# Kernel tuning notes

Hardware: AMD Instinct MI355X
Metric: run time of the kernel (lower is better)

The kernel has to match this reference:

```python
import jax, jax.numpy as jnp
import numpy as np
from jax import lax

DEPTH = 3
KS = 5

def haar_fwd(x):
    # x: (B, 2h, 2w, C) -> (B, h, w, C, 4) with bands [LL, LH, HL, HH]
    a = x[:, 0::2, 0::2]; b = x[:, 0::2, 1::2]
    c = x[:, 1::2, 0::2]; d = x[:, 1::2, 1::2]
    ll = (a + b + c + d) * 0.5
    lh = (a + b - c - d) * 0.5
    hl = (a - b + c - d) * 0.5
    hh = (a - b - c + d) * 0.5
    return jnp.stack([ll, lh, hl, hh], axis=-1)

def haar_inv(co):
    # co: (B, h, w, C, 4) -> (B, 2h, 2w, C); orthonormal inverse of haar_fwd
    ll, lh, hl, hh = co[..., 0], co[..., 1], co[..., 2], co[..., 3]
    a = (ll + lh + hl + hh) * 0.5
    b = (ll + lh - hl - hh) * 0.5
    c = (ll - lh + hl - hh) * 0.5
    d = (ll - lh - hl + hh) * 0.5
    B, h, w, C = ll.shape
    top = jnp.stack([a, b], axis=3).reshape(B, h, 2 * w, C)
    bot = jnp.stack([c, d], axis=3).reshape(B, h, 2 * w, C)
    return jnp.stack([top, bot], axis=2).reshape(B, 2 * h, 2 * w, C)

def depthwise(x, k, groups):
    return lax.conv_general_dilated(
        x, k, (1, 1), 'SAME',
        dimension_numbers=('NHWC', 'HWIO', 'NHWC'),
        feature_group_count=groups)

def setup_inputs() -> dict:
    key = jax.random.key(0)
    ks = jax.random.split(key, 2 + DEPTH)
    B, H, W, C = 8, 256, 256, 128
    x = jax.random.normal(ks[0], (B, H, W, C), jnp.float32)
    fan = float(KS * KS)
    base_kernel = jax.random.normal(ks[1], (KS, KS, 1, C), jnp.float32) / np.sqrt(fan)
    base_bias = jnp.zeros((C,), jnp.float32)
    base_scale = jnp.ones((1, 1, 1, C), jnp.float32)
    wavelet_kernels = tuple(
        jax.random.normal(ks[2 + i], (KS, KS, 1, C * 4), jnp.float32) / np.sqrt(fan)
        for i in range(DEPTH))
    wavelet_scales = tuple(jnp.full((1, 1, 1, C * 4), 0.1, jnp.float32) for _ in range(DEPTH))
    return dict(x=x, base_kernel=base_kernel, base_bias=base_bias, base_scale=base_scale,
                wavelet_kernels=wavelet_kernels, wavelet_scales=wavelet_scales)

def reference(x, base_kernel, base_bias, base_scale, wavelet_kernels, wavelet_scales):
    B, H, W, C = x.shape
    # pad input to even H/W (edge mode); no-op for even dims
    xp = jnp.pad(x, ((0, 0), (0, H % 2), (0, W % 2), (0, 0)), mode='edge')
    # multi-level Haar forward: level l decomposes the raw LL of level l-1
    coeffs, dims = [], []
    cur = xp
    for _ in range(DEPTH):
        _, h, w, _ = cur.shape
        dims.append((h, w))
        cur = jnp.pad(cur, ((0, 0), (0, h % 2), (0, w % 2), (0, 0)), mode='edge')
        co = haar_fwd(cur)
        coeffs.append(co)
        cur = co[..., 0]
    # per-level depthwise conv with scale fused into the kernel
    conv_coeffs = []
    for lvl in range(DEPTH):
        co = coeffs[lvl]
        Bc, h, w, Cc, _ = co.shape
        flat = co.reshape(Bc, h, w, Cc * 4)
        fused = wavelet_scales[lvl] * wavelet_kernels[lvl]  # (KS,KS,1,4C)
        out = depthwise(flat, fused, Cc * 4)
        conv_coeffs.append(out.reshape(Bc, h, w, Cc, 4))
    # inverse reconstruction with add of deeper reconstruction into LL band
    next_ll = jnp.zeros_like(conv_coeffs[-1][..., 0])
    for lvl in range(DEPTH - 1, -1, -1):
        co = conv_coeffs[lvl].at[..., 0].add(next_ll)
        rec = haar_inv(co)
        h, w = dims[lvl]
        next_ll = rec[:, :h, :w, :]
    output_wt = next_ll[:, :H, :W, :]
    x_base = base_scale * (depthwise(xp, base_kernel, C) + base_bias)[:, :H, :W, :]
    return x_base + output_wt
```

## Files before the change

kernel.cpp:

```cpp
#include <hip/hip_runtime.h>

#define NC 128
#define NB 8
#define CPB 32

__device__ __forceinline__ float4 ld4(const float* p) { return *(const float4*)p; }
__device__ __forceinline__ float4 add4(float4 a, float4 b) {
    return make_float4(a.x + b.x, a.y + b.y, a.z + b.z, a.w + b.w);
}
__device__ __forceinline__ float4 sub4(float4 a, float4 b) {
    return make_float4(a.x - b.x, a.y - b.y, a.z - b.z, a.w - b.w);
}
__device__ __forceinline__ float4 muls4(float4 a, float s) {
    return make_float4(a.x * s, a.y * s, a.z * s, a.w * s);
}
__device__ __forceinline__ float4 fma4(float4 a, float4 w, float4 c) {
    return make_float4(fmaf(a.x, w.x, c.x), fmaf(a.y, w.y, c.y),
                       fmaf(a.z, w.z, c.z), fmaf(a.w, w.w, c.w));
}

__global__ __launch_bounds__(256) void k_haar_ll(
    const float* __restrict__ P, float* __restrict__ out, int h, int w)
{
    int idx = blockIdx.x * blockDim.x + threadIdx.x;
    int total = NB * h * w * (NC / 4);
    if (idx >= total) return;
    int cq = idx & (NC / 4 - 1);
    int t  = idx / (NC / 4);
    int j  = t % w; t /= w;
    int i  = t % h;
    int b  = t / h;
    size_t W2C  = (size_t)(2 * w) * NC;
    size_t base = (((size_t)b * (2 * h) + 2 * i) * (2 * w) + 2 * j) * NC + cq * 4;
    float4 A  = *(const float4*)(P + base);
    float4 Bv = *(const float4*)(P + base + NC);
    float4 Cv = *(const float4*)(P + base + W2C);
    float4 Dv = *(const float4*)(P + base + W2C + NC);
    float4 r;
    r.x = (A.x + Bv.x + Cv.x + Dv.x) * 0.5f;
    r.y = (A.y + Bv.y + Cv.y + Dv.y) * 0.5f;
    r.z = (A.z + Bv.z + Cv.z + Dv.z) * 0.5f;
    r.w = (A.w + Bv.w + Cv.w + Dv.w) * 0.5f;
    *(float4*)(out + (size_t)idx * 4) = r;
}

#define WL4(s, t)  (wl + ((s) * 25 + (t)) * CPB + 4 * tc)
#define WB4(m, n)  (wbase + ((m) * 5 + (n)) * CPB + 4 * tc)

template <bool BASE, int RR>
__global__ __launch_bounds__(256) void k_convinv(
    const float* __restrict__ P, const float* __restrict__ nll,
    const float* __restrict__ wk, const float* __restrict__ wsc,
    const float* __restrict__ bk, const float* __restrict__ bb,
    const float* __restrict__ bs, float* __restrict__ out,
    int h, int w)
{
    extern __shared__ float lds[];
    float* wl     = lds;
    float* wbase  = wl + 4 * 25 * CPB;
    float* bscale = wbase + 25 * CPB;
    float* bbias  = bscale + CPB;

    const int cg    = blockIdx.x & 3;
    const int jtile = blockIdx.x >> 2;
    const int c0    = cg * CPB;
    const int tid   = threadIdx.x + threadIdx.y * 8;

    for (int u = tid; u < 4 * 25 * CPB; u += 256) {
        int tcc = u & (CPB - 1);
        int st  = u / CPB;
        int t   = st % 25;
        int s   = st / 25;
        wl[u] = 0.5f * wsc[(c0 + tcc) * 4 + s] * wk[t * (4 * NC) + (c0 + tcc) * 4 + s];
    }
    if (BASE) {
        for (int u = tid; u < 25 * CPB; u += 256) {
            int tcc = u & (CPB - 1);
            int t   = u / CPB;
            wbase[u] = bk[t * NC + c0 + tcc];
        }
        if (tid < CPB) { bscale[tid] = bs[c0 + tid]; bbias[tid] = bb[c0 + tid]; }
    }
    __syncthreads();

    const int tc = threadIdx.x;
    const int cc = c0 + 4 * tc;
    const int b  = blockIdx.z;
    const int i  = blockIdx.y;
    const int ja = jtile * (32 * RR) + threadIdx.y * RR;
    if (ja >= w) return;
    const int PH = 2 * h;
    const size_t rowC = (size_t)(2 * w) * NC;

    int   coff[RR + 4];
    float cmask[RR + 4];
    #pragma unroll
    for (int q = 0; q < RR + 4; ++q) {
        int xq  = ja + q - 2;
        int xqc = min(max(xq, 0), w - 1);
        coff[q]  = xqc * (2 * NC);
        cmask[q] = (xq >= 0 && xq < w) ? 1.f : 0.f;
    }

    float4 acc0[RR], acc1[RR], acc2[RR], acc3[RR];
    float4 b00[RR], b01[RR], b10[RR], b11[RR];
    #pragma unroll
    for (int s = 0; s < RR; ++s) {
        acc0[s] = acc1[s] = acc2[s] = acc3[s] = make_float4(0.f, 0.f, 0.f, 0.f);
        b00[s] = b01[s] = b10[s] = b11[s] = make_float4(0.f, 0.f, 0.f, 0.f);
    }

    #pragma unroll
    for (int ky = 0; ky < 5; ++ky) {
        int y = i + ky - 2;
        if (y < 0 || y >= h) continue;
        const float* prA = P + ((size_t)b * PH + 2 * y) * rowC + cc;
        const float* prC = prA + rowC;
        #pragma unroll
        for (int q = 0; q < RR + 4; ++q) {
            float m = cmask[q];
            const float* pA = prA + coff[q];
            const float* pC = prC + coff[q];
            float4 A  = muls4(ld4(pA), m);
            float4 Bv = muls4(ld4(pA + NC), m);
            float4 Cv = muls4(ld4(pC), m);
            float4 Dv = muls4(ld4(pC + NC), m);
            float4 sA = add4(A, Bv), sC = add4(Cv, Dv);
            float4 dA = sub4(A, Bv), dC = sub4(Cv, Dv);
            float4 s0 = add4(sA, sC), s1 = sub4(sA, sC);
            float4 s2 = add4(dA, dC), s3 = sub4(dA, dC);
            #pragma unroll
            for (int s = 0; s < RR; ++s) {
                const int kx = q - s;
                if (kx < 0 || kx > 4) continue;
                const int t = ky * 5 + kx;
                acc0[s] = fma4(s0, ld4(WL4(0, t)), acc0[s]);
                acc1[s] = fma4(s1, ld4(WL4(1, t)), acc1[s]);
                acc2[s] = fma4(s2, ld4(WL4(2, t)), acc2[s]);
                acc3[s] = fma4(s3, ld4(WL4(3, t)), acc3[s]);
                if (BASE && ky >= 1 && ky <= 3 && kx >= 1 && kx <= 3) {
                    b00[s] = fma4(A, ld4(WB4(2 * ky - 2, 2 * kx - 2)), b00[s]);
                    if (kx >= 2)            b01[s] = fma4(A,  ld4(WB4(2 * ky - 2, 2 * kx - 3)), b01[s]);
                    if (ky >= 2)            b10[s] = fma4(A,  ld4(WB4(2 * ky - 3, 2 * kx - 2)), b10[s]);
                    if (ky >= 2 && kx >= 2) b11[s] = fma4(A,  ld4(WB4(2 * ky - 3, 2 * kx - 3)), b11[s]);
                    if (kx <= 2)            b00[s] = fma4(Bv, ld4(WB4(2 * ky - 2, 2 * kx - 1)), b00[s]);
                                            b01[s] = fma4(Bv, ld4(WB4(2 * ky - 2, 2 * kx - 2)), b01[s]);
                    if (ky >= 2 && kx <= 2) b10[s] = fma4(Bv, ld4(WB4(2 * ky - 3, 2 * kx - 1)), b10[s]);
                    if (ky >= 2)            b11[s] = fma4(Bv, ld4(WB4(2 * ky - 3, 2 * kx - 2)), b11[s]);
                    if (ky <= 2)            b00[s] = fma4(Cv, ld4(WB4(2 * ky - 1, 2 * kx - 2)), b00[s]);
                    if (ky <= 2 && kx >= 2) b01[s] = fma4(Cv, ld4(WB4(2 * ky - 1, 2 * kx - 3)), b01[s]);
                                            b10[s] = fma4(Cv, ld4(WB4(2 * ky - 2, 2 * kx - 2)), b10[s]);
                    if (kx >= 2)            b11[s] = fma4(Cv, ld4(WB4(2 * ky - 2, 2 * kx - 3)), b11[s]);
                    if (ky <= 2 && kx <= 2) b00[s] = fma4(Dv, ld4(WB4(2 * ky - 1, 2 * kx - 1)), b00[s]);
                    if (ky <= 2)            b01[s] = fma4(Dv, ld4(WB4(2 * ky - 1, 2 * kx - 2)), b01[s]);
                    if (kx <= 2)            b10[s] = fma4(Dv, ld4(WB4(2 * ky - 2, 2 * kx - 1)), b10[s]);
                                            b11[s] = fma4(Dv, ld4(WB4(2 * ky - 2, 2 * kx - 2)), b11[s]);
                }
            }
        }
    }

    #pragma unroll
    for (int s = 0; s < RR; ++s) {
        int j = ja + s;
        if (j >= w) break;
        float4 a0 = acc0[s];
        if (nll) a0 = add4(a0, ld4(nll + (((size_t)b * h + i) * w + j) * NC + cc));
        float4 av = muls4(add4(add4(a0, acc1[s]), add4(acc2[s], acc3[s])), 0.5f);
        float4 bv = muls4(sub4(add4(a0, acc1[s]), add4(acc2[s], acc3[s])), 0.5f);
        float4 cv = muls4(add4(sub4(a0, acc1[s]), sub4(acc2[s], acc3[s])), 0.5f);
        float4 dv = muls4(sub4(sub4(a0, acc1[s]), sub4(acc2[s], acc3[s])), 0.5f);

        size_t ob = ((size_t)b * PH + 2 * i) * rowC + (size_t)(2 * j) * NC + cc;
        if (BASE) {
            float4 sc = ld4(bscale + 4 * tc);
            float4 bi = ld4(bbias + 4 * tc);
            float4 o00 = make_float4(sc.x * (b00[s].x + bi.x), sc.y * (b00[s].y + bi.y),
                                     sc.z * (b00[s].z + bi.z), sc.w * (b00[s].w + bi.w));
            float4 o01 = make_float4(sc.x * (b01[s].x + bi.x), sc.y * (b01[s].y + bi.y),
                                     sc.z * (b01[s].z + bi.z), sc.w * (b01[s].w + bi.w));
            float4 o10 = make_float4(sc.x * (b10[s].x + bi.x), sc.y * (b10[s].y + bi.y),
                                     sc.z * (b10[s].z + bi.z), sc.w * (b10[s].w + bi.w));
            float4 o11 = make_float4(sc.x * (b11[s].x + bi.x), sc.y * (b11[s].y + bi.y),
                                     sc.z * (b11[s].z + bi.z), sc.w * (b11[s].w + bi.w));
            *(float4*)(out + ob)             = add4(o00, av);
            *(float4*)(out + ob + NC)        = add4(o01, bv);
            *(float4*)(out + ob + rowC)      = add4(o10, cv);
            *(float4*)(out + ob + rowC + NC) = add4(o11, dv);
        } else {
            *(float4*)(out + ob)             = av;
            *(float4*)(out + ob + NC)        = bv;
            *(float4*)(out + ob + rowC)      = cv;
            *(float4*)(out + ob + rowC + NC) = dv;
        }
    }
}

extern "C" void kernel_launch(void* const* d_in, const int* in_sizes, int n_in,
                              void* d_out, int out_size, void* d_ws, size_t ws_size,
                              hipStream_t stream)
{
    const float* x  = (const float*)d_in[0];
    const float* bk = (const float*)d_in[1];
    const float* bb = (const float*)d_in[2];
    const float* bs = (const float*)d_in[3];
    const float* wk[3];
    const float* wv[3];
    if (n_in >= 10) {
        for (int i = 0; i < 3; ++i) {
            wk[i] = (const float*)d_in[4 + i];
            wv[i] = (const float*)d_in[7 + i];
        }
    } else {
        const float* wkc = (const float*)d_in[4];
        const float* wvc = (const float*)d_in[5];
        for (int i = 0; i < 3; ++i) {
            wk[i] = wkc + (size_t)i * 25 * 4 * NC;
            wv[i] = wvc + (size_t)i * 4 * NC;
        }
    }
    float* out = (float*)d_out;

    float* ll0 = out;
    float* ll1 = out + 16777216;
    float* r2  = out + 16777216 + 4194304;
    float* r1  = (float*)d_ws;

    {
        int total = NB * 128 * 128 * (NC / 4);
        k_haar_ll<<<(total + 255) / 256, 256, 0, stream>>>(x, ll0, 128, 128);
    }
    {
        int total = NB * 64 * 64 * (NC / 4);
        k_haar_ll<<<(total + 255) / 256, 256, 0, stream>>>(ll0, ll1, 64, 64);
    }

    size_t lds_nb = (size_t)(4 * 25 * CPB) * sizeof(float);
    size_t lds_b  = (size_t)(4 * 25 * CPB + 25 * CPB + 2 * CPB) * sizeof(float);
    dim3 blk(8, 32);

    k_convinv<false, 1><<<dim3(4, 32, NB), blk, lds_nb, stream>>>(
        ll1, nullptr, wk[2], wv[2], nullptr, nullptr, nullptr, r2, 32, 32);

    k_convinv<false, 2><<<dim3(4, 64, NB), blk, lds_nb, stream>>>(
        ll0, r2, wk[1], wv[1], nullptr, nullptr, nullptr, r1, 64, 64);

    k_convinv<true, 1><<<dim3(4 * 4, 128, NB), blk, lds_b, stream>>>(
        x, r1, wk[0], wv[0], bk, bb, bs, out, 128, 128);
}
```

Before: 567.0 us.

## Split base depthwise conv out of fused level-0 wavelet kernel

Removes the base 5x5 depthwise convolution from the level-0 conv+inverse-Haar kernel and runs it as a separate k_base kernel that reads x and accumulates into the output in place. The fused kernel no longer carries sixteen extra accumulators and the conditional FMA tree, so register pressure drops, and the level-0 launch now processes two columns per thread (RR=2). The cost is an extra full read and write of the output plus a second pass over x.

```diff
diff --git a/kernel.cpp b/kernel.cpp
--- a/kernel.cpp
+++ b/kernel.cpp
@@ -45,21 +45,15 @@
 }
 
 #define WL4(s, t)  (wl + ((s) * 25 + (t)) * CPB + 4 * tc)
-#define WB4(m, n)  (wbase + ((m) * 5 + (n)) * CPB + 4 * tc)
-
-template <bool BASE, int RR>
+
+template <int RR>
 __global__ __launch_bounds__(256) void k_convinv(
     const float* __restrict__ P, const float* __restrict__ nll,
     const float* __restrict__ wk, const float* __restrict__ wsc,
-    const float* __restrict__ bk, const float* __restrict__ bb,
-    const float* __restrict__ bs, float* __restrict__ out,
-    int h, int w)
+    float* __restrict__ out, int h, int w)
 {
     extern __shared__ float lds[];
-    float* wl     = lds;
-    float* wbase  = wl + 4 * 25 * CPB;
-    float* bscale = wbase + 25 * CPB;
-    float* bbias  = bscale + CPB;
+    float* wl = lds;
 
     const int cg    = blockIdx.x & 3;
     const int jtile = blockIdx.x >> 2;
@@ -72,14 +66,6 @@
         int t   = st % 25;
         int s   = st / 25;
         wl[u] = 0.5f * wsc[(c0 + tcc) * 4 + s] * wk[t * (4 * NC) + (c0 + tcc) * 4 + s];
-    }
-    if (BASE) {
-        for (int u = tid; u < 25 * CPB; u += 256) {
-            int tcc = u & (CPB - 1);
-            int t   = u / CPB;
-            wbase[u] = bk[t * NC + c0 + tcc];
-        }
-        if (tid < CPB) { bscale[tid] = bs[c0 + tid]; bbias[tid] = bb[c0 + tid]; }
     }
     __syncthreads();
 
@@ -103,12 +89,9 @@
     }
 
     float4 acc0[RR], acc1[RR], acc2[RR], acc3[RR];
-    float4 b00[RR], b01[RR], b10[RR], b11[RR];
-    #pragma unroll
-    for (int s = 0; s < RR; ++s) {
+    #pragma unroll
+    for (int s = 0; s < RR; ++s)
         acc0[s] = acc1[s] = acc2[s] = acc3[s] = make_float4(0.f, 0.f, 0.f, 0.f);
-        b00[s] = b01[s] = b10[s] = b11[s] = make_float4(0.f, 0.f, 0.f, 0.f);
-    }
 
     #pragma unroll
     for (int ky = 0; ky < 5; ++ky) {
@@ -138,24 +121,6 @@
                 acc1[s] = fma4(s1, ld4(WL4(1, t)), acc1[s]);
                 acc2[s] = fma4(s2, ld4(WL4(2, t)), acc2[s]);
                 acc3[s] = fma4(s3, ld4(WL4(3, t)), acc3[s]);
-                if (BASE && ky >= 1 && ky <= 3 && kx >= 1 && kx <= 3) {
-                    b00[s] = fma4(A, ld4(WB4(2 * ky - 2, 2 * kx - 2)), b00[s]);
-                    if (kx >= 2)            b01[s] = fma4(A,  ld4(WB4(2 * ky - 2, 2 * kx - 3)), b01[s]);
-                    if (ky >= 2)            b10[s] = fma4(A,  ld4(WB4(2 * ky - 3, 2 * kx - 2)), b10[s]);
-                    if (ky >= 2 && kx >= 2) b11[s] = fma4(A,  ld4(WB4(2 * ky - 3, 2 * kx - 3)), b11[s]);
-                    if (kx <= 2)            b00[s] = fma4(Bv, ld4(WB4(2 * ky - 2, 2 * kx - 1)), b00[s]);
-                                            b01[s] = fma4(Bv, ld4(WB4(2 * ky - 2, 2 * kx - 2)), b01[s]);
-                    if (ky >= 2 && kx <= 2) b10[s] = fma4(Bv, ld4(WB4(2 * ky - 3, 2 * kx - 1)), b10[s]);
-                    if (ky >= 2)            b11[s] = fma4(Bv, ld4(WB4(2 * ky - 3, 2 * kx - 2)), b11[s]);
-                    if (ky <= 2)            b00[s] = fma4(Cv, ld4(WB4(2 * ky - 1, 2 * kx - 2)), b00[s]);
-                    if (ky <= 2 && kx >= 2) b01[s] = fma4(Cv, ld4(WB4(2 * ky - 1, 2 * kx - 3)), b01[s]);
-                                            b10[s] = fma4(Cv, ld4(WB4(2 * ky - 2, 2 * kx - 2)), b10[s]);
-                    if (kx >= 2)            b11[s] = fma4(Cv, ld4(WB4(2 * ky - 2, 2 * kx - 3)), b11[s]);
-                    if (ky <= 2 && kx <= 2) b00[s] = fma4(Dv, ld4(WB4(2 * ky - 1, 2 * kx - 1)), b00[s]);
-                    if (ky <= 2)            b01[s] = fma4(Dv, ld4(WB4(2 * ky - 1, 2 * kx - 2)), b01[s]);
-                    if (kx <= 2)            b10[s] = fma4(Dv, ld4(WB4(2 * ky - 2, 2 * kx - 1)), b10[s]);
-                                            b11[s] = fma4(Dv, ld4(WB4(2 * ky - 2, 2 * kx - 2)), b11[s]);
-                }
             }
         }
     }
@@ -172,28 +137,75 @@
         float4 dv = muls4(sub4(sub4(a0, acc1[s]), sub4(acc2[s], acc3[s])), 0.5f);
 
         size_t ob = ((size_t)b * PH + 2 * i) * rowC + (size_t)(2 * j) * NC + cc;
-        if (BASE) {
-            float4 sc = ld4(bscale + 4 * tc);
-            float4 bi = ld4(bbias + 4 * tc);
-            float4 o00 = make_float4(sc.x * (b00[s].x + bi.x), sc.y * (b00[s].y + bi.y),
-                                     sc.z * (b00[s].z + bi.z), sc.w * (b00[s].w + bi.w));
-            float4 o01 = make_float4(sc.x * (b01[s].x + bi.x), sc.y * (b01[s].y + bi.y),
-                                     sc.z * (b01[s].z + bi.z), sc.w * (b01[s].w + bi.w));
-            float4 o10 = make_float4(sc.x * (b10[s].x + bi.x), sc.y * (b10[s].y + bi.y),
-                                     sc.z * (b10[s].z + bi.z), sc.w * (b10[s].w + bi.w));
-            float4 o11 = make_float4(sc.x * (b11[s].x + bi.x), sc.y * (b11[s].y + bi.y),
-                                     sc.z * (b11[s].z + bi.z), sc.w * (b11[s].w + bi.w));
-            *(float4*)(out + ob)             = add4(o00, av);
-            *(float4*)(out + ob + NC)        = add4(o01, bv);
-            *(float4*)(out + ob + rowC)      = add4(o10, cv);
-            *(float4*)(out + ob + rowC + NC) = add4(o11, dv);
-        } else {
-            *(float4*)(out + ob)             = av;
-            *(float4*)(out + ob + NC)        = bv;
-            *(float4*)(out + ob + rowC)      = cv;
-            *(float4*)(out + ob + rowC + NC) = dv;
-        }
-    }
+        *(float4*)(out + ob)             = av;
+        *(float4*)(out + ob + NC)        = bv;
+        *(float4*)(out + ob + rowC)      = cv;
+        *(float4*)(out + ob + rowC + NC) = dv;
+    }
+}
+
+__global__ __launch_bounds__(256) void k_base(
+    const float* __restrict__ x, const float* __restrict__ bk,
+    const float* __restrict__ bb, const float* __restrict__ bs,
+    float* __restrict__ out, int H, int W)
+{
+    extern __shared__ float lds[];
+    float* wb     = lds;
+    float* bscale = wb + 25 * CPB;
+    float* bbias  = bscale + CPB;
+
+    const int cg    = blockIdx.x & 3;
+    const int jtile = blockIdx.x >> 2;
+    const int c0    = cg * CPB;
+    const int tid   = threadIdx.x + threadIdx.y * 8;
+
+    for (int u = tid; u < 25 * CPB; u += 256) {
+        int tcc = u & (CPB - 1);
+        int t   = u / CPB;
+        wb[u] = bk[t * NC + c0 + tcc];
+    }
+    if (tid < CPB) { bscale[tid] = bs[c0 + tid]; bbias[tid] = bb[c0 + tid]; }
+    __syncthreads();
+
+    const int tc = threadIdx.x;
+    const int cc = c0 + 4 * tc;
+    const int b  = blockIdx.z;
+    const int p  = blockIdx.y;
+    const int q  = jtile * 32 + threadIdx.y;
+    const size_t rowC = (size_t)W * NC;
+
+    int   coff[5];
+    float cm[5];
+    #pragma unroll
+    for (int n = 0; n < 5; ++n) {
+        int xq  = q + n - 2;
+        int xqc = min(max(xq, 0), W - 1);
+        coff[n] = xqc * NC;
+        cm[n]   = (xq >= 0 && xq < W) ? 1.f : 0.f;
+    }
+
+    float4 acc = make_float4(0.f, 0.f, 0.f, 0.f);
+    #pragma unroll
+    for (int m = 0; m < 5; ++m) {
+        int y = p + m - 2;
+        if (y < 0 || y >= H) continue;
+        const float* xr = x + ((size_t)b * H + y) * rowC + cc;
+        #pragma unroll
+        for (int n = 0; n < 5; ++n) {
+            float4 v = muls4(ld4(xr + coff[n]), cm[n]);
+            acc = fma4(v, ld4(wb + (m * 5 + n) * CPB + 4 * tc), acc);
+        }
+    }
+
+    float4 sc = ld4(bscale + 4 * tc);
+    float4 bi = ld4(bbias + 4 * tc);
+    size_t ob = ((size_t)b * H + p) * rowC + (size_t)q * NC + cc;
+    float4 o  = ld4(out + ob);
+    o.x += sc.x * (acc.x + bi.x);
+    o.y += sc.y * (acc.y + bi.y);
+    o.z += sc.z * (acc.z + bi.z);
+    o.w += sc.w * (acc.w + bi.w);
+    *(float4*)(out + ob) = o;
 }
 
 extern "C" void kernel_launch(void* const* d_in, const int* in_sizes, int n_in,
@@ -235,16 +247,19 @@
         k_haar_ll<<<(total + 255) / 256, 256, 0, stream>>>(ll0, ll1, 64, 64);
     }
 
-    size_t lds_nb = (size_t)(4 * 25 * CPB) * sizeof(float);
-    size_t lds_b  = (size_t)(4 * 25 * CPB + 25 * CPB + 2 * CPB) * sizeof(float);
+    size_t lds_w = (size_t)(4 * 25 * CPB) * sizeof(float);
+    size_t lds_b = (size_t)(25 * CPB + 2 * CPB) * sizeof(float);
     dim3 blk(8, 32);
 
-    k_convinv<false, 1><<<dim3(4, 32, NB), blk, lds_nb, stream>>>(
-        ll1, nullptr, wk[2], wv[2], nullptr, nullptr, nullptr, r2, 32, 32);
-
-    k_convinv<false, 2><<<dim3(4, 64, NB), blk, lds_nb, stream>>>(
-        ll0, r2, wk[1], wv[1], nullptr, nullptr, nullptr, r1, 64, 64);
-
-    k_convinv<true, 1><<<dim3(4 * 4, 128, NB), blk, lds_b, stream>>>(
-        x, r1, wk[0], wv[0], bk, bb, bs, out, 128, 128);
-}
+    k_convinv<1><<<dim3(4, 32, NB), blk, lds_w, stream>>>(
+        ll1, nullptr, wk[2], wv[2], r2, 32, 32);
+
+    k_convinv<2><<<dim3(4, 64, NB), blk, lds_w, stream>>>(
+        ll0, r2, wk[1], wv[1], r1, 64, 64);
+
+    k_convinv<2><<<dim3(2 * 4, 128, NB), blk, lds_w, stream>>>(
+        x, r1, wk[0], wv[0], out, 128, 128);
+
+    k_base<<<dim3((256 / 32) * 4, 256, NB), blk, lds_b, stream>>>(
+        x, bk, bb, bs, out, 256, 256);
+}
```

Result: slower. 725.1 us (+27.9%).
